# Kernel optimization log

Hardware: AMD Instinct MI355X
Metric: run time of the kernel (lower is better)

The kernel has to match this reference:

```python
import jax, jax.numpy as jnp
import numpy as np

L, B, S, D, H, E = 3, 2, 2048, 1024, 16, 4
Dh = D // H  # 64
DF = E * D   # 4096


def _ln(x, g, b, eps=1e-5):
    m = jnp.mean(x, axis=-1, keepdims=True)
    v = jnp.mean(jnp.square(x - m), axis=-1, keepdims=True)
    return (x - m) * jax.lax.rsqrt(v + eps) * g + b


def setup_inputs() -> dict:
    key = jax.random.key(0)
    ks = jax.random.split(key, 12)
    s = 0.02
    f32 = jnp.float32
    return {
        "x":    jax.random.normal(ks[0], (B, S, D), f32),
        "Wq":   jax.random.normal(ks[1], (L, Dh, Dh), f32) * s,
        "Wk":   jax.random.normal(ks[2], (L, Dh, Dh), f32) * s,
        "Wv":   jax.random.normal(ks[3], (L, Dh, Dh), f32) * s,
        "Wo":   jax.random.normal(ks[4], (L, D, D), f32) * s,
        "bo":   jnp.zeros((L, D), f32),
        "ln1_g": jnp.ones((L, D), f32),
        "ln1_b": jnp.zeros((L, D), f32),
        "W1":   jax.random.normal(ks[5], (L, DF, D), f32) * s,
        "b1":   jnp.zeros((L, DF), f32),
        "W2":   jax.random.normal(ks[6], (L, D, DF), f32) * s,
        "b2":   jnp.zeros((L, D), f32),
        "ln2_g": jnp.ones((L, D), f32),
        "ln2_b": jnp.zeros((L, D), f32),
    }


def reference(x, Wq, Wk, Wv, Wo, bo, ln1_g, ln1_b, W1, b1, W2, b2, ln2_g, ln2_b):
    scale = 1.0 / np.sqrt(Dh).astype(np.float32)
    out = x
    for l in range(L):
        xh = out.reshape(B, S, H, Dh)
        # per-head Linear (shared 64x64 weight across heads), torch Linear: y = x @ W.T
        q = jnp.einsum('bshd,ed->bhse', xh, Wq[l])  # [B,H,S,Dh]
        k = jnp.einsum('bshd,ed->bhse', xh, Wk[l])
        v = jnp.einsum('bshd,ed->bhse', xh, Wv[l])
        att = jax.nn.softmax(jnp.einsum('bhse,bhte->bhst', q, k) * scale, axis=-1)
        ctx = jnp.einsum('bhst,bhtd->bshd', att, v).reshape(B, S, D)
        att_out = ctx @ Wo[l].T + bo[l]
        n1 = _ln(att_out + out, ln1_g[l], ln1_b[l])  # residual adds layer input (v == out)
        ff = jax.nn.relu(n1 @ W1[l].T + b1[l]) @ W2[l].T + b2[l]
        out = _ln(ff + n1, ln2_g[l], ln2_b[l])
    return out
```

## Files before the change

### kernel.cpp

```cpp
#include <hip/hip_runtime.h>
#include <hip/hip_bf16.h>
#include <math.h>


#define DEVINL __device__ __forceinline__
typedef unsigned short ushort_t;
using short8 = __attribute__((ext_vector_type(8))) short;
using f32x4  = __attribute__((ext_vector_type(4))) float;

#if defined(__has_builtin)
#if __has_builtin(__builtin_amdgcn_exp2f)
#define EXPFN(x) __builtin_amdgcn_exp2f(x)
#define QSCALE 0.18033688011112042f
#define HAVE_EXP2 1
#endif
#endif
#ifndef HAVE_EXP2
#define EXPFN(x) __expf(x)
#define QSCALE 0.125f
#endif

DEVINL short f2b(float f) {
  unsigned u = __float_as_uint(f);
  u += 0x7fff + ((u >> 16) & 1);
  return (short)(u >> 16);
}
DEVINL unsigned pk2(float a, float b) {
  unsigned ua = __float_as_uint(a), ub = __float_as_uint(b);
  ua += 0x7fff + ((ua >> 16) & 1);
  ub += 0x7fff + ((ub >> 16) & 1);
  return (ua >> 16) | (ub & 0xffff0000u);
}
DEVINL unsigned pkc(float a, float b) {
  float2 f; f.x = a; f.y = b;
  __hip_bfloat162 h = __float22bfloat162_rn(f);
  return *reinterpret_cast<unsigned*>(&h);
}
DEVINL f32x4 mfma16(short8 a, short8 b, f32x4 c) {
  return __builtin_amdgcn_mfma_f32_16x16x32_bf16(a, b, c, 0, 0, 0);
}

typedef __attribute__((address_space(3))) void lds_void;
typedef __attribute__((address_space(1))) void gbl_void;
DEVINL void gl16(const void* g, void* l) {
  __builtin_amdgcn_global_load_lds((const gbl_void*)(unsigned long long)g,
                                   (lds_void*)(unsigned long long)l, 16, 0, 0);
}

__global__ __launch_bounds__(256)
void conv_bf16(const float* __restrict__ src, ushort_t* __restrict__ dst,
               int n8) {
  int i = blockIdx.x * 256 + threadIdx.x;
  const int stride = gridDim.x * 256;
  for (; i < n8; i += stride) {
    float4 a = ((const float4*)src)[2 * i];
    float4 b = ((const float4*)src)[2 * i + 1];
    uint4 o;
    o.x = pk2(a.x, a.y); o.y = pk2(a.z, a.w);
    o.z = pk2(b.x, b.y); o.w = pk2(b.z, b.w);
    ((uint4*)dst)[i] = o;
  }
}

DEVINL float block_sum(float v, float* red) {
#pragma unroll
  for (int off = 32; off > 0; off >>= 1) v += __shfl_xor(v, off, 64);
  if ((threadIdx.x & 63) == 0) red[threadIdx.x >> 6] = v;
  __syncthreads();
  float r = red[0] + red[1] + red[2] + red[3];
  __syncthreads();
  return r;
}

__global__ __launch_bounds__(256)
void ln_dual2(const float* __restrict__ pa, const float* __restrict__ pb,
              const float* __restrict__ bias, const float* __restrict__ R,
              const float* __restrict__ g, const float* __restrict__ b,
              float* __restrict__ outf, ushort_t* __restrict__ outb) {
  __shared__ float red[4];
  const size_t base = (size_t)blockIdx.x * 1024 + threadIdx.x * 4;
  float4 va = *(const float4*)(pa + base);
  float4 vb = *(const float4*)(pb + base);
  float4 vr = *(const float4*)(R + base);
  float4 vbi = *(const float4*)(bias + threadIdx.x * 4);
  float4 v;
  v.x = va.x + vb.x + vr.x + vbi.x;
  v.y = va.y + vb.y + vr.y + vbi.y;
  v.z = va.z + vb.z + vr.z + vbi.z;
  v.w = va.w + vb.w + vr.w + vbi.w;
  float s = block_sum(v.x + v.y + v.z + v.w, red);
  float mean = s * (1.0f / 1024.0f);
  float dx = v.x - mean, dy = v.y - mean, dz = v.z - mean, dw = v.w - mean;
  float sq = block_sum(dx * dx + dy * dy + dz * dz + dw * dw, red);
  float rstd = rsqrtf(sq * (1.0f / 1024.0f) + 1e-5f);
  const float4 gv = *(const float4*)(g + threadIdx.x * 4);
  const float4 bv = *(const float4*)(b + threadIdx.x * 4);
  float4 o;
  o.x = dx * rstd * gv.x + bv.x;
  o.y = dy * rstd * gv.y + bv.y;
  o.z = dz * rstd * gv.z + bv.z;
  o.w = dw * rstd * gv.w + bv.w;
  *(float4*)(outf + base) = o;
  uint2 p;
  p.x = pk2(o.x, o.y); p.y = pk2(o.z, o.w);
  *(uint2*)(outb + base) = p;
}

template <int BM, int BN, int WR, int WC, bool OBF, int EPI, bool SWZ>
__global__ __launch_bounds__(WR * WC * 64)
void gemm_db(const ushort_t* __restrict__ A, const ushort_t* __restrict__ W,
             const float* __restrict__ bias, void* __restrict__ Cp, int M,
             int N, int Klen, int lda, int ldw) {
  constexpr int THREADS = WR * WC * 64;
  constexpr int FM = BM / WR / 16;
  constexpr int FN = BN / WC / 16;
  constexpr int CA = BM * 8 / THREADS;
  constexpr int CB = BN * 8 / THREADS;
  __shared__ __align__(16) ushort_t As[2][BM * 64];
  __shared__ __align__(16) ushort_t Bs[2][BN * 64];
  const int tid = threadIdx.x;
  const int lane = tid & 63, lo = lane & 15, hi = lane >> 4, w = tid >> 6;
  int bx = blockIdx.x, by = blockIdx.y;
  if (SWZ) {
    int id = by * gridDim.x + bx;
    const int cpx = (gridDim.x * gridDim.y) >> 3;
    id = (id & 7) * cpx + (id >> 3);
    bx = id % gridDim.x;
    by = id / gridDim.x;
  }
  const int m0 = by * BM, n0 = bx * BN;
  const int wm = (w / WC) * (BM / WR), wn = (w % WC) * (BN / WC);
  const int kbase = blockIdx.z * Klen;

  auto stage = [&](int t, int buf) {
    const int k0 = kbase + t * 64;
#pragma unroll
    for (int i = 0; i < CA; ++i) {
      const int c = i * THREADS + tid;
      const int r = c >> 3, sg = (c & 7) ^ (r & 7);
      gl16(A + (size_t)(m0 + r) * lda + k0 + sg * 8, &As[buf][c * 8]);
    }
#pragma unroll
    for (int i = 0; i < CB; ++i) {
      const int c = i * THREADS + tid;
      const int r = c >> 3, sg = (c & 7) ^ (r & 7);
      gl16(W + (size_t)(n0 + r) * ldw + k0 + sg * 8, &Bs[buf][c * 8]);
    }
  };

  f32x4 acc[FM][FN] = {};
  const int nt = Klen / 64;
  stage(0, 0);
  for (int t = 0; t < nt; ++t) {
    const int cur = t & 1;
    __syncthreads();
    if (t + 1 < nt) stage(t + 1, cur ^ 1);
#pragma unroll
    for (int ks = 0; ks < 2; ++ks) {
      short8 af[FM], bf[FN];
#pragma unroll
      for (int fm = 0; fm < FM; ++fm) {
        const int row = wm + fm * 16 + lo;
        af[fm] = *(const short8*)
            &As[cur][row * 64 + (((ks * 4 + hi) ^ (row & 7)) << 3)];
      }
#pragma unroll
      for (int fn = 0; fn < FN; ++fn) {
        const int row = wn + fn * 16 + lo;
        bf[fn] = *(const short8*)
            &Bs[cur][row * 64 + (((ks * 4 + hi) ^ (row & 7)) << 3)];
      }
#pragma unroll
      for (int fm = 0; fm < FM; ++fm)
#pragma unroll
        for (int fn = 0; fn < FN; ++fn)
          acc[fm][fn] = mfma16(af[fm], bf[fn], acc[fm][fn]);
    }
  }

  float bv[FN];
#pragma unroll
  for (int fn = 0; fn < FN; ++fn)
    bv[fn] = (EPI & 1) ? bias[n0 + wn + fn * 16 + lo] : 0.f;
  float* Cf = (float*)Cp + (size_t)blockIdx.z * M * N;
#pragma unroll
  for (int fm = 0; fm < FM; ++fm)
#pragma unroll
    for (int fn = 0; fn < FN; ++fn) {
      const int col = n0 + wn + fn * 16 + lo;
#pragma unroll
      for (int r = 0; r < 4; ++r) {
        const int row = m0 + wm + fm * 16 + hi * 4 + r;
        float v = acc[fm][fn][r] + bv[fn];
        if (EPI & 4) v = fmaxf(v, 0.f);
        if (OBF)
          ((ushort_t*)Cp)[(size_t)row * N + col] = (ushort_t)f2b(v);
        else
          Cf[(size_t)row * N + col] = v;
      }
    }
}

__global__ __launch_bounds__(256)
void qkv_kernel(const ushort_t* __restrict__ A, const ushort_t* __restrict__ Wq,
                const ushort_t* __restrict__ Wk, const ushort_t* __restrict__ Wv,
                ushort_t* __restrict__ q, ushort_t* __restrict__ k,
                ushort_t* __restrict__ v) {
  __shared__ __align__(16) ushort_t As[128 * 64];
  __shared__ __align__(16) ushort_t Ws[3][64 * 64];
  const int tid = threadIdx.x;
  const int lane = tid & 63, lo = lane & 15, hi = lane >> 4, w = tid >> 6;
  const int m0 = blockIdx.x * 128;
  const int wm = (w >> 1) * 64, wn = (w & 1) * 32;

#pragma unroll
  for (int i = 0; i < 4; ++i) {
    const int c = i * 256 + tid;
    const int r = c >> 3, sg = (c & 7) ^ (r & 7);
    gl16(A + (size_t)(m0 + r) * 64 + sg * 8, As + c * 8);
  }
#pragma unroll
  for (int o = 0; o < 3; ++o) {
    const ushort_t* wb = (o == 0) ? Wq : (o == 1) ? Wk : Wv;
#pragma unroll
    for (int i = 0; i < 2; ++i) {
      const int c = i * 256 + tid;
      const int r = c >> 3, sg = (c & 7) ^ (r & 7);
      gl16(wb + (size_t)r * 64 + sg * 8, Ws[o] + c * 8);
    }
  }
  __syncthreads();

#pragma unroll
  for (int o = 0; o < 3; ++o) {
    ushort_t* ob = (o == 0) ? q : (o == 1) ? k : v;
    const float sc = (o == 0) ? QSCALE : 1.0f;
    f32x4 acc[4][2] = {};
#pragma unroll
    for (int ks = 0; ks < 2; ++ks) {
      short8 af[4], bf[2];
#pragma unroll
      for (int fm = 0; fm < 4; ++fm) {
        const int row = wm + fm * 16 + lo;
        af[fm] = *(const short8*)
            &As[row * 64 + (((ks * 4 + hi) ^ (row & 7)) << 3)];
      }
#pragma unroll
      for (int fn = 0; fn < 2; ++fn) {
        const int row = wn + fn * 16 + lo;
        bf[fn] = *(const short8*)
            &Ws[o][row * 64 + (((ks * 4 + hi) ^ (row & 7)) << 3)];
      }
#pragma unroll
      for (int fm = 0; fm < 4; ++fm)
#pragma unroll
        for (int fn = 0; fn < 2; ++fn)
          acc[fm][fn] = mfma16(af[fm], bf[fn], acc[fm][fn]);
    }
#pragma unroll
    for (int fm = 0; fm < 4; ++fm)
#pragma unroll
      for (int fn = 0; fn < 2; ++fn) {
        const int col = wn + fn * 16 + lo;
#pragma unroll
        for (int r = 0; r < 4; ++r) {
          const int row = m0 + wm + fm * 16 + hi * 4 + r;
          size_t idx;
          if (o == 2) {
            idx = (size_t)row * 64 + col;
          } else {
            idx = (size_t)((row >> 15) * 16 + (row & 15)) * 131072 +
                  (size_t)((row >> 4) & 2047) * 64 + col;
          }
          ob[idx] = (ushort_t)f2b(acc[fm][fn][r] * sc);
        }
      }
  }
}

__global__ __launch_bounds__(256)
void vtrans(const ushort_t* __restrict__ V, ushort_t* __restrict__ VT) {
  __shared__ ushort_t T[64][65];
  const int tid = threadIdx.x;
  const int s0 = blockIdx.x * 64, hd0 = blockIdx.y * 64, b = blockIdx.z;
  const ushort_t* src = V + (size_t)b * 2097152;
  ushort_t* dst = VT + (size_t)b * 2097152;
#pragma unroll
  for (int i = 0; i < 2; ++i) {
    int c = tid + i * 256;
    int s = c >> 3, kg = c & 7;
    short8 hv = *(const short8*)(src + (size_t)(s0 + s) * 1024 + hd0 + kg * 8);
#pragma unroll
    for (int j = 0; j < 8; ++j) T[s][kg * 8 + j] = (ushort_t)hv[j];
  }
  __syncthreads();
#pragma unroll
  for (int i = 0; i < 2; ++i) {
    int c = tid + i * 256;
    int hd = c >> 3, sg = c & 7;
    short8 o;
#pragma unroll
    for (int j = 0; j < 8; ++j) o[j] = (short)T[sg * 8 + j][hd];
    *(short8*)(dst + (size_t)(hd0 + hd) * 2048 + s0 + sg * 8) = o;
  }
}

__global__ __launch_bounds__(256)
void attn3(const ushort_t* __restrict__ Qh, const ushort_t* __restrict__ Kh,
           const ushort_t* __restrict__ VT, ushort_t* __restrict__ O) {
  __shared__ __align__(16) ushort_t Kbuf[2][64 * 64];
  __shared__ __align__(16) ushort_t Vbuf[2][64 * 64];
  __shared__ __align__(16) ushort_t Pbuf[4][16 * 40];
  const int tid = threadIdx.x, w = tid >> 6, lane = tid & 63;
  const int lo = lane & 15, hi = lane >> 4;
  const int bh = blockIdx.y, b = bh >> 4, h = bh & 15;
  const size_t hq = (size_t)bh * 131072;
  const size_t vth = (size_t)b * 2097152 + (size_t)h * 131072;
  const size_t oh = (size_t)b * 2097152 + (size_t)h * 64;
  const int qrow = blockIdx.x * 64 + w * 16;
  ushort_t* Pw = Pbuf[w];

  const ushort_t* qp = Qh + hq + (size_t)(qrow + lo) * 64 + hi * 8;
  const short8 qf0 = *(const short8*)qp;
  const short8 qf1 = *(const short8*)(qp + 32);

  const int c0 = tid, c1 = 256 + tid;
  const int r0 = c0 >> 3, s0 = ((c0 & 7) ^ (r0 & 7)) << 3;
  const int r1 = c1 >> 3, s1 = ((c1 & 7) ^ (r1 & 7)) << 3;
  const ushort_t* kg0 = Kh + hq + (size_t)r0 * 64 + s0;
  const ushort_t* kg1 = Kh + hq + (size_t)r1 * 64 + s1;
  const ushort_t* vg0 = VT + vth + (size_t)r0 * 2048 + s0;
  const ushort_t* vg1 = VT + vth + (size_t)r1 * 2048 + s1;

  auto stage = [&](int kt, int buf) {
    gl16(kg0 + (size_t)kt * 4096, &Kbuf[buf][c0 * 8]);
    gl16(kg1 + (size_t)kt * 4096, &Kbuf[buf][c1 * 8]);
    gl16(vg0 + kt * 64, &Vbuf[buf][c0 * 8]);
    gl16(vg1 + kt * 64, &Vbuf[buf][c1 * 8]);
  };

  f32x4 acc[4] = {};
  f32x4 lacc = {};
  const int sw = lo & 7;
  const int ko0 = (hi ^ sw) << 3, ko1 = ((4 + hi) ^ sw) << 3;

  auto body = [&](const ushort_t* Kc, const ushort_t* Vc) {
    f32x4 sc[4];
#pragma unroll
    for (int fm = 0; fm < 4; ++fm) {
      const int rb = (fm * 16 + lo) * 64;
      f32x4 t = {};
      t = mfma16(*(const short8*)&Kc[rb + ko0], qf0, t);
      t = mfma16(*(const short8*)&Kc[rb + ko1], qf1, t);
      sc[fm] = t;
    }
    short8 vf[4][2];
#pragma unroll
    for (int fn = 0; fn < 4; ++fn) {
      const int rb = (fn * 16 + lo) * 64;
      vf[fn][0] = *(const short8*)&Vc[rb + ko0];
      vf[fn][1] = *(const short8*)&Vc[rb + ko1];
    }
#pragma unroll
    for (int fm = 0; fm < 4; ++fm) {
      f32x4 p;
      p[0] = EXPFN(sc[fm][0]); p[1] = EXPFN(sc[fm][1]);
      p[2] = EXPFN(sc[fm][2]); p[3] = EXPFN(sc[fm][3]);
      lacc += p;
      uint2 pw;
      pw.x = pkc(p[0], p[1]); pw.y = pkc(p[2], p[3]);
      *(uint2*)&Pw[lo * 40 + fm * 16 + hi * 4] = pw;
    }
    short8 pb0 = *(const short8*)&Pw[lo * 40 + hi * 8];
    short8 pb1 = *(const short8*)&Pw[lo * 40 + 32 + hi * 8];
#pragma unroll
    for (int fn = 0; fn < 4; ++fn) {
      acc[fn] = mfma16(vf[fn][0], pb0, acc[fn]);
      acc[fn] = mfma16(vf[fn][1], pb1, acc[fn]);
    }
  };

  stage(0, 0);
  __syncthreads();
  for (int kt2 = 0; kt2 < 16; ++kt2) {
    const int kt = kt2 * 2;
    stage(kt + 1, 1);
    body(Kbuf[0], Vbuf[0]);
    __syncthreads();
    if (kt2 < 15) stage(kt + 2, 0);
    body(Kbuf[1], Vbuf[1]);
    __syncthreads();
  }

  float lsum = (lacc[0] + lacc[1]) + (lacc[2] + lacc[3]);
  lsum += __shfl_xor(lsum, 16);
  lsum += __shfl_xor(lsum, 32);
  const float inv = 1.0f / lsum;
  ushort_t* op = O + oh + (size_t)(qrow + lo) * 1024 + hi * 4;
#pragma unroll
  for (int fn = 0; fn < 4; ++fn) {
    uint2 o;
    o.x = pk2(acc[fn][0] * inv, acc[fn][1] * inv);
    o.y = pk2(acc[fn][2] * inv, acc[fn][3] * inv);
    *(uint2*)(op + fn * 16) = o;
  }
}

extern "C" void kernel_launch(void* const* d_in, const int* in_sizes, int n_in,
                              void* d_out, int out_size, void* d_ws,
                              size_t ws_size, hipStream_t stream) {
  const float* x    = (const float*)d_in[0];
  const float* Wq   = (const float*)d_in[1];
  const float* Wk   = (const float*)d_in[2];
  const float* Wv   = (const float*)d_in[3];
  const float* Wo   = (const float*)d_in[4];
  const float* bo   = (const float*)d_in[5];
  const float* ln1g = (const float*)d_in[6];
  const float* ln1b = (const float*)d_in[7];
  const float* W1   = (const float*)d_in[8];
  const float* b1   = (const float*)d_in[9];
  const float* W2   = (const float*)d_in[10];
  const float* b2   = (const float*)d_in[11];
  const float* ln2g = (const float*)d_in[12];
  const float* ln2b = (const float*)d_in[13];
  float* out = (float*)d_out;
  char* wsb = (char*)d_ws;

  float*    t0a = (float*)wsb;
  float*    t0b = (float*)(wsb + (16ull << 20));
  ushort_t* q   = (ushort_t*)(wsb + (32ull << 20));
  ushort_t* k   = (ushort_t*)(wsb + (40ull << 20));
  ushort_t* v   = (ushort_t*)(wsb + (48ull << 20));
  ushort_t* vt  = (ushort_t*)(wsb + (56ull << 20));
  ushort_t* ff  = q;
  ushort_t* ctx = (ushort_t*)(wsb + (64ull << 20));
  ushort_t* n1b = ctx;
  ushort_t* xbf = (ushort_t*)(wsb + (72ull << 20));
  ushort_t* wqb = (ushort_t*)(wsb + (80ull << 20));
  ushort_t* wkb = wqb + 3 * 4096;
  ushort_t* wvb = wkb + 3 * 4096;
  ushort_t* wob = (ushort_t*)(wsb + (81ull << 20));
  ushort_t* w1b = (ushort_t*)(wsb + (83ull << 20));
  ushort_t* w2b = (ushort_t*)(wsb + (91ull << 20));

  auto conv = [&](const float* s, ushort_t* d, long n) {
    int n8 = (int)(n / 8);
    int g = (n8 + 255) / 256;
    if (g > 2048) g = 2048;
    conv_bf16<<<g, 256, 0, stream>>>(s, d, n8);
  };
  conv(x, xbf, 4194304);
  conv(Wq, wqb, 3 * 4096);
  conv(Wk, wkb, 3 * 4096);
  conv(Wv, wvb, 3 * 4096);

  const ushort_t* curb = xbf;
  const float* curf = x;
  for (int l = 0; l < 3; ++l) {
    conv(Wo + (size_t)l * 1048576, wob, 1048576);
    conv(W1 + (size_t)l * 4194304, w1b, 4194304);
    conv(W2 + (size_t)l * 4194304, w2b, 4194304);

    qkv_kernel<<<512, 256, 0, stream>>>(curb, wqb + l * 4096, wkb + l * 4096,
                                        wvb + l * 4096, q, k, v);
    vtrans<<<dim3(32, 16, 2), 256, 0, stream>>>(v, vt);
    attn3<<<dim3(32, 32), 256, 0, stream>>>(q, k, vt, ctx);
    gemm_db<128, 64, 2, 2, false, 0, true>
        <<<dim3(16, 32, 2), 256, 0, stream>>>(ctx, wob, nullptr, t0a, 4096,
                                              1024, 512, 1024, 1024);
    ln_dual2<<<4096, 256, 0, stream>>>(t0a, t0b, bo + l * 1024, curf,
                                       ln1g + l * 1024, ln1b + l * 1024, out,
                                       n1b);
    gemm_db<256, 128, 2, 4, true, 5, true>
        <<<dim3(32, 16, 1), 512, 0, stream>>>(n1b, w1b, b1 + l * 4096, ff,
                                              4096, 4096, 1024, 1024, 1024);
    gemm_db<128, 64, 2, 2, false, 0, true>
        <<<dim3(16, 32, 2), 256, 0, stream>>>(ff, w2b, nullptr, t0a, 4096,
                                              1024, 2048, 4096, 4096);
    ln_dual2<<<4096, 256, 0, stream>>>(t0a, t0b, b2 + l * 1024, out,
                                       ln2g + l * 1024, ln2b + l * 1024, out,
                                       xbf);
    curb = xbf;
    curf = out;
  }
}
```

Measured before the change: 631.8 us.

## Store split-K partials in bf16, rework GEMM and attention pipelining, retile FFN1

Split-K GEMM partial outputs are now written as bf16 instead of fp32, and the layernorm kernel reads bf16 partials, which cuts intermediate traffic but rounds the partial sums. The GEMM main loop is restructured: each stage is issued before explicit vmcnt waits and raw barriers. Attention moves to a three-buffer K/V pipeline with raised wave priority around the MFMA sections. The FFN1 GEMM is retiled from 256x128 with 512 threads to 128x128 with 256 threads and more blocks.

```diff
diff --git a/kernel.cpp b/kernel.cpp
--- a/kernel.cpp
+++ b/kernel.cpp
@@ -36,6 +36,8 @@
   __hip_bfloat162 h = __float22bfloat162_rn(f);
   return *reinterpret_cast<unsigned*>(&h);
 }
+DEVINL float bl(unsigned u) { return __uint_as_float(u << 16); }
+DEVINL float bh(unsigned u) { return __uint_as_float(u & 0xffff0000u); }
 DEVINL f32x4 mfma16(short8 a, short8 b, f32x4 c) {
   return __builtin_amdgcn_mfma_f32_16x16x32_bf16(a, b, c, 0, 0, 0);
 }
@@ -46,6 +48,11 @@
   __builtin_amdgcn_global_load_lds((const gbl_void*)(unsigned long long)g,
                                    (lds_void*)(unsigned long long)l, 16, 0, 0);
 }
+template <int N> DEVINL void waitvm() {
+  asm volatile("s_waitcnt vmcnt(%0)" ::"n"(N) : "memory");
+}
+DEVINL void barrier_raw() { __builtin_amdgcn_s_barrier(); }
+DEVINL void sched0() { __builtin_amdgcn_sched_barrier(0); }
 
 __global__ __launch_bounds__(256)
 void conv_bf16(const float* __restrict__ src, ushort_t* __restrict__ dst,
@@ -73,21 +80,21 @@
 }
 
 __global__ __launch_bounds__(256)
-void ln_dual2(const float* __restrict__ pa, const float* __restrict__ pb,
+void ln_dual2(const ushort_t* __restrict__ pa, const ushort_t* __restrict__ pb,
               const float* __restrict__ bias, const float* __restrict__ R,
               const float* __restrict__ g, const float* __restrict__ b,
               float* __restrict__ outf, ushort_t* __restrict__ outb) {
   __shared__ float red[4];
   const size_t base = (size_t)blockIdx.x * 1024 + threadIdx.x * 4;
-  float4 va = *(const float4*)(pa + base);
-  float4 vb = *(const float4*)(pb + base);
+  uint2 ua = *(const uint2*)(pa + base);
+  uint2 ub = *(const uint2*)(pb + base);
   float4 vr = *(const float4*)(R + base);
   float4 vbi = *(const float4*)(bias + threadIdx.x * 4);
   float4 v;
-  v.x = va.x + vb.x + vr.x + vbi.x;
-  v.y = va.y + vb.y + vr.y + vbi.y;
-  v.z = va.z + vb.z + vr.z + vbi.z;
-  v.w = va.w + vb.w + vr.w + vbi.w;
+  v.x = bl(ua.x) + bl(ub.x) + vr.x + vbi.x;
+  v.y = bh(ua.x) + bh(ub.x) + vr.y + vbi.y;
+  v.z = bl(ua.y) + bl(ub.y) + vr.z + vbi.z;
+  v.w = bh(ua.y) + bh(ub.y) + vr.w + vbi.w;
   float s = block_sum(v.x + v.y + v.z + v.w, red);
   float mean = s * (1.0f / 1024.0f);
   float dx = v.x - mean, dy = v.y - mean, dz = v.z - mean, dw = v.w - mean;
@@ -116,6 +123,7 @@
   constexpr int FN = BN / WC / 16;
   constexpr int CA = BM * 8 / THREADS;
   constexpr int CB = BN * 8 / THREADS;
+  constexpr int L = CA + CB;
   __shared__ __align__(16) ushort_t As[2][BM * 64];
   __shared__ __align__(16) ushort_t Bs[2][BN * 64];
   const int tid = threadIdx.x;
@@ -149,15 +157,10 @@
   };
 
   f32x4 acc[FM][FN] = {};
-  const int nt = Klen / 64;
-  stage(0, 0);
-  for (int t = 0; t < nt; ++t) {
-    const int cur = t & 1;
-    __syncthreads();
-    if (t + 1 < nt) stage(t + 1, cur ^ 1);
+  auto compute = [&](int cur) {
 #pragma unroll
     for (int ks = 0; ks < 2; ++ks) {
-      short8 af[FM], bf[FN];
+      short8 af[FM], bf_[FN];
 #pragma unroll
       for (int fm = 0; fm < FM; ++fm) {
         const int row = wm + fm * 16 + lo;
@@ -167,22 +170,35 @@
 #pragma unroll
       for (int fn = 0; fn < FN; ++fn) {
         const int row = wn + fn * 16 + lo;
-        bf[fn] = *(const short8*)
+        bf_[fn] = *(const short8*)
             &Bs[cur][row * 64 + (((ks * 4 + hi) ^ (row & 7)) << 3)];
       }
 #pragma unroll
       for (int fm = 0; fm < FM; ++fm)
 #pragma unroll
         for (int fn = 0; fn < FN; ++fn)
-          acc[fm][fn] = mfma16(af[fm], bf[fn], acc[fm][fn]);
-    }
-  }
+          acc[fm][fn] = mfma16(af[fm], bf_[fn], acc[fm][fn]);
+    }
+  };
+
+  const int nt = Klen / 64;
+  stage(0, 0);
+  for (int t = 0; t < nt - 1; ++t) {
+    const int cur = t & 1;
+    stage(t + 1, cur ^ 1);
+    waitvm<L>();
+    barrier_raw(); sched0();
+    compute(cur);
+    barrier_raw(); sched0();
+  }
+  waitvm<0>();
+  barrier_raw(); sched0();
+  compute((nt - 1) & 1);
 
   float bv[FN];
 #pragma unroll
   for (int fn = 0; fn < FN; ++fn)
     bv[fn] = (EPI & 1) ? bias[n0 + wn + fn * 16 + lo] : 0.f;
-  float* Cf = (float*)Cp + (size_t)blockIdx.z * M * N;
 #pragma unroll
   for (int fm = 0; fm < FM; ++fm)
 #pragma unroll
@@ -193,10 +209,13 @@
         const int row = m0 + wm + fm * 16 + hi * 4 + r;
         float v = acc[fm][fn][r] + bv[fn];
         if (EPI & 4) v = fmaxf(v, 0.f);
-        if (OBF)
-          ((ushort_t*)Cp)[(size_t)row * N + col] = (ushort_t)f2b(v);
-        else
+        if (OBF) {
+          ushort_t* Cb = (ushort_t*)Cp + (size_t)blockIdx.z * M * N;
+          Cb[(size_t)row * N + col] = (ushort_t)f2b(v);
+        } else {
+          float* Cf = (float*)Cp + (size_t)blockIdx.z * M * N;
           Cf[(size_t)row * N + col] = v;
+        }
       }
     }
 }
@@ -308,8 +327,8 @@
 __global__ __launch_bounds__(256)
 void attn3(const ushort_t* __restrict__ Qh, const ushort_t* __restrict__ Kh,
            const ushort_t* __restrict__ VT, ushort_t* __restrict__ O) {
-  __shared__ __align__(16) ushort_t Kbuf[2][64 * 64];
-  __shared__ __align__(16) ushort_t Vbuf[2][64 * 64];
+  __shared__ __align__(16) ushort_t Kbuf[3][64 * 64];
+  __shared__ __align__(16) ushort_t Vbuf[3][64 * 64];
   __shared__ __align__(16) ushort_t Pbuf[4][16 * 40];
   const int tid = threadIdx.x, w = tid >> 6, lane = tid & 63;
   const int lo = lane & 15, hi = lane >> 4;
@@ -332,11 +351,11 @@
   const ushort_t* vg0 = VT + vth + (size_t)r0 * 2048 + s0;
   const ushort_t* vg1 = VT + vth + (size_t)r1 * 2048 + s1;
 
-  auto stage = [&](int kt, int buf) {
-    gl16(kg0 + (size_t)kt * 4096, &Kbuf[buf][c0 * 8]);
-    gl16(kg1 + (size_t)kt * 4096, &Kbuf[buf][c1 * 8]);
-    gl16(vg0 + kt * 64, &Vbuf[buf][c0 * 8]);
-    gl16(vg1 + kt * 64, &Vbuf[buf][c1 * 8]);
+  auto stage = [&](int kt, ushort_t* Kd, ushort_t* Vd) {
+    gl16(kg0 + (size_t)kt * 4096, Kd + c0 * 8);
+    gl16(kg1 + (size_t)kt * 4096, Kd + c1 * 8);
+    gl16(vg0 + kt * 64, Vd + c0 * 8);
+    gl16(vg1 + kt * 64, Vd + c1 * 8);
   };
 
   f32x4 acc[4] = {};
@@ -346,6 +365,7 @@
 
   auto body = [&](const ushort_t* Kc, const ushort_t* Vc) {
     f32x4 sc[4];
+    __builtin_amdgcn_s_setprio(1);
 #pragma unroll
     for (int fm = 0; fm < 4; ++fm) {
       const int rb = (fm * 16 + lo) * 64;
@@ -354,6 +374,7 @@
       t = mfma16(*(const short8*)&Kc[rb + ko1], qf1, t);
       sc[fm] = t;
     }
+    __builtin_amdgcn_s_setprio(0);
     short8 vf[4][2];
 #pragma unroll
     for (int fn = 0; fn < 4; ++fn) {
@@ -373,24 +394,31 @@
     }
     short8 pb0 = *(const short8*)&Pw[lo * 40 + hi * 8];
     short8 pb1 = *(const short8*)&Pw[lo * 40 + 32 + hi * 8];
+    __builtin_amdgcn_s_setprio(1);
 #pragma unroll
     for (int fn = 0; fn < 4; ++fn) {
       acc[fn] = mfma16(vf[fn][0], pb0, acc[fn]);
       acc[fn] = mfma16(vf[fn][1], pb1, acc[fn]);
     }
+    __builtin_amdgcn_s_setprio(0);
   };
 
-  stage(0, 0);
-  __syncthreads();
-  for (int kt2 = 0; kt2 < 16; ++kt2) {
-    const int kt = kt2 * 2;
-    stage(kt + 1, 1);
-    body(Kbuf[0], Vbuf[0]);
-    __syncthreads();
-    if (kt2 < 15) stage(kt + 2, 0);
-    body(Kbuf[1], Vbuf[1]);
-    __syncthreads();
-  }
+  ushort_t *kA = Kbuf[0], *kB = Kbuf[1], *kC = Kbuf[2];
+  ushort_t *vA = Vbuf[0], *vB = Vbuf[1], *vC = Vbuf[2];
+  stage(0, kA, vA);
+  stage(1, kB, vB);
+  for (int kt = 0; kt < 31; ++kt) {
+    waitvm<4>();
+    barrier_raw(); sched0();
+    if (kt < 30) stage(kt + 2, kC, vC);
+    body(kA, vA);
+    ushort_t* t;
+    t = kA; kA = kB; kB = kC; kC = t;
+    t = vA; vA = vB; vB = vC; vC = t;
+  }
+  waitvm<0>();
+  barrier_raw(); sched0();
+  body(kA, vA);
 
   float lsum = (lacc[0] + lacc[1]) + (lacc[2] + lacc[3]);
   lsum += __shfl_xor(lsum, 16);
@@ -426,22 +454,22 @@
   float* out = (float*)d_out;
   char* wsb = (char*)d_ws;
 
-  float*    t0a = (float*)wsb;
-  float*    t0b = (float*)(wsb + (16ull << 20));
-  ushort_t* q   = (ushort_t*)(wsb + (32ull << 20));
-  ushort_t* k   = (ushort_t*)(wsb + (40ull << 20));
-  ushort_t* v   = (ushort_t*)(wsb + (48ull << 20));
-  ushort_t* vt  = (ushort_t*)(wsb + (56ull << 20));
+  ushort_t* t0  = (ushort_t*)wsb;
+  ushort_t* t0b = t0 + 4194304;
+  ushort_t* q   = (ushort_t*)(wsb + (16ull << 20));
+  ushort_t* k   = (ushort_t*)(wsb + (24ull << 20));
+  ushort_t* v   = (ushort_t*)(wsb + (32ull << 20));
+  ushort_t* vt  = (ushort_t*)(wsb + (40ull << 20));
   ushort_t* ff  = q;
-  ushort_t* ctx = (ushort_t*)(wsb + (64ull << 20));
+  ushort_t* ctx = (ushort_t*)(wsb + (48ull << 20));
   ushort_t* n1b = ctx;
-  ushort_t* xbf = (ushort_t*)(wsb + (72ull << 20));
-  ushort_t* wqb = (ushort_t*)(wsb + (80ull << 20));
+  ushort_t* xbf = (ushort_t*)(wsb + (56ull << 20));
+  ushort_t* wqb = (ushort_t*)(wsb + (64ull << 20));
   ushort_t* wkb = wqb + 3 * 4096;
   ushort_t* wvb = wkb + 3 * 4096;
-  ushort_t* wob = (ushort_t*)(wsb + (81ull << 20));
-  ushort_t* w1b = (ushort_t*)(wsb + (83ull << 20));
-  ushort_t* w2b = (ushort_t*)(wsb + (91ull << 20));
+  ushort_t* wob = (ushort_t*)(wsb + (65ull << 20));
+  ushort_t* w1b = (ushort_t*)(wsb + (67ull << 20));
+  ushort_t* w2b = (ushort_t*)(wsb + (75ull << 20));
 
   auto conv = [&](const float* s, ushort_t* d, long n) {
     int n8 = (int)(n / 8);
@@ -465,19 +493,19 @@
                                         wvb + l * 4096, q, k, v);
     vtrans<<<dim3(32, 16, 2), 256, 0, stream>>>(v, vt);
     attn3<<<dim3(32, 32), 256, 0, stream>>>(q, k, vt, ctx);
-    gemm_db<128, 64, 2, 2, false, 0, true>
-        <<<dim3(16, 32, 2), 256, 0, stream>>>(ctx, wob, nullptr, t0a, 4096,
+    gemm_db<128, 64, 2, 2, true, 0, true>
+        <<<dim3(16, 32, 2), 256, 0, stream>>>(ctx, wob, nullptr, t0, 4096,
                                               1024, 512, 1024, 1024);
-    ln_dual2<<<4096, 256, 0, stream>>>(t0a, t0b, bo + l * 1024, curf,
+    ln_dual2<<<4096, 256, 0, stream>>>(t0, t0b, bo + l * 1024, curf,
                                        ln1g + l * 1024, ln1b + l * 1024, out,
                                        n1b);
-    gemm_db<256, 128, 2, 4, true, 5, true>
-        <<<dim3(32, 16, 1), 512, 0, stream>>>(n1b, w1b, b1 + l * 4096, ff,
+    gemm_db<128, 128, 2, 2, true, 5, true>
+        <<<dim3(32, 32, 1), 256, 0, stream>>>(n1b, w1b, b1 + l * 4096, ff,
                                               4096, 4096, 1024, 1024, 1024);
-    gemm_db<128, 64, 2, 2, false, 0, true>
-        <<<dim3(16, 32, 2), 256, 0, stream>>>(ff, w2b, nullptr, t0a, 4096,
+    gemm_db<128, 64, 2, 2, true, 0, true>
+        <<<dim3(16, 32, 2), 256, 0, stream>>>(ff, w2b, nullptr, t0, 4096,
                                               1024, 2048, 4096, 4096);
-    ln_dual2<<<4096, 256, 0, stream>>>(t0a, t0b, b2 + l * 1024, out,
+    ln_dual2<<<4096, 256, 0, stream>>>(t0, t0b, b2 + l * 1024, out,
                                        ln2g + l * 1024, ln2b + l * 1024, out,
                                        xbf);
     curb = xbf;
```

New measurement: 635.5 us. No clear change (+0.6%).
